# Optimization experiments

Measured on AMD Instinct MI355X. Metric: run time of the kernel, lower is better.

Reference implementation:

```python
import jax, jax.numpy as jnp
import numpy as np

B, S, E, H = 2, 2048, 1024, 16
D = E // H  # head dim = 64


def setup_inputs() -> dict:
    key = jax.random.key(0)
    ks = jax.random.split(key, 9)
    sc = 0.02
    return {
        "inputs": jax.random.normal(ks[0], (B, S, E), jnp.float32),
        "Wq": jax.random.normal(ks[1], (E, E), jnp.float32) * sc,
        "bq": jnp.zeros((E,), jnp.float32),
        "Wk": jax.random.normal(ks[2], (E, E), jnp.float32) * sc,
        "bk": jnp.zeros((E,), jnp.float32),
        "Wv": jax.random.normal(ks[3], (E, E), jnp.float32) * sc,
        "bv": jnp.zeros((E,), jnp.float32),
        "Wo": jax.random.normal(ks[4], (E, E), jnp.float32) * sc,
        "bo": jnp.zeros((E,), jnp.float32),
    }


def _split_heads(x):
    # [B, S, E] -> [B, H, S, D]
    b, s, _ = x.shape
    return x.reshape(b, s, H, D).transpose(0, 2, 1, 3)


def reference(inputs, Wq, bq, Wk, bk, Wv, bv, Wo, bo):
    q = _split_heads(inputs @ Wq + bq)
    k = _split_heads(inputs @ Wk + bk)
    v = _split_heads(inputs @ Wv + bv)

    # scaled dot-product scores: [B, H, S, S]
    score = jnp.einsum("bhqd,bhkd->bhqk", q, k) / jnp.sqrt(jnp.float32(D))

    # causal mask, exactly as the original: score*mask - 10000*(1-mask)
    i = jnp.arange(S)[:, None]
    j = jnp.arange(S)[None, :]
    mask = (i >= j).astype(score.dtype)  # square case of i >= j - S + S
    score = score * mask - 10000.0 * (1.0 - mask)

    weights = jax.nn.softmax(score, axis=-1)
    attn = jnp.einsum("bhqk,bhkd->bhqd", weights, v)  # [B, H, S, D]
    attn = attn.transpose(0, 2, 1, 3).reshape(inputs.shape[0], S, E)
    return attn @ Wo + bo
```

## Files before the change

### kernel.cpp

```cpp
#include <hip/hip_runtime.h>
#include <stdint.h>

#define Bc 2
#define Sc 2048
#define Ec 1024
#define Hc 16
#define Dc 64
#define Mc (Bc*Sc)

typedef __attribute__((ext_vector_type(4))) float f32x4;
typedef __attribute__((ext_vector_type(8))) short bf16x8v;

#define SCL 0.1803368801f

__device__ __forceinline__ unsigned short f2bf(float f){
  unsigned int u = __float_as_uint(f);
  u += 0x7FFFu + ((u >> 16) & 1u);
  return (unsigned short)(u >> 16);
}

#define GLDS(src, dst) __builtin_amdgcn_global_load_lds( \
    (const __attribute__((address_space(1))) void*)(src), \
    (__attribute__((address_space(3))) void*)(dst), 16, 0, 0)

__global__ __launch_bounds__(256) void k_prep(const float* __restrict__ X,
                                              unsigned short* __restrict__ Xb,
                                              const float* __restrict__ W0, const float* __restrict__ W1,
                                              const float* __restrict__ W2, const float* __restrict__ W3,
                                              unsigned short* __restrict__ WT4){
  __shared__ float st[64][65];
  int bx = blockIdx.x, t = threadIdx.x;
  if (bx < 4096){
    int i = bx*256 + t;
    float4 v = ((const float4*)X)[i];
    ushort4 o;
    o.x = f2bf(v.x); o.y = f2bf(v.y); o.z = f2bf(v.z); o.w = f2bf(v.w);
    ((ushort4*)Xb)[i] = o;
  } else {
    int id = bx - 4096;
    int z = id >> 8, rem = id & 255;
    int k0 = (rem >> 4)*64, n0 = (rem & 15)*64;
    const float* W = (z==0)?W0 : (z==1)?W1 : (z==2)?W2 : W3;
    unsigned short* o = WT4 + (size_t)z * Ec * Ec;
    #pragma unroll
    for (int i=0;i<16;i++){ int lin=i*256+t; int r=lin>>6, c=lin&63;
      st[r][c] = W[(size_t)(k0+r)*Ec + n0+c]; }
    __syncthreads();
    #pragma unroll
    for (int i=0;i<16;i++){ int lin=i*256+t; int nn=lin>>6, kk=lin&63;
      o[(size_t)(n0+nn)*Ec + k0+kk] = f2bf(st[kk][nn]); }
  }
}

__global__ __launch_bounds__(256,2) void k_qkv(const unsigned short* __restrict__ A,
                                               const unsigned short* __restrict__ WT4,
                                               const float* __restrict__ bq,
                                               const float* __restrict__ bk,
                                               const float* __restrict__ bv,
                                               unsigned short* __restrict__ QKV){
  __shared__ unsigned short sA[2][128*64];
  __shared__ unsigned short sB[2][3][64*64];
  int bm = blockIdx.y, bn = blockIdx.x;
  int t = threadIdx.x, w = t>>6, lane = t&63, quad = lane>>4, m16 = lane&15;
  int wm = w>>1, wn = w&1, sw = m16 & 7;
  f32x4 acc[3][4][2];
  #pragma unroll
  for (int z=0;z<3;z++)
    #pragma unroll
    for (int i=0;i<4;i++)
      #pragma unroll
      for (int j=0;j<2;j++) acc[z][i][j] = (f32x4){0.f,0.f,0.f,0.f};

  auto stage = [&](int kt, int buf){
    #pragma unroll
    for (int i=0;i<4;i++){
      int cb = (w*4 + i)*64;
      int L = cb + lane;
      int row = L>>3, c = (L&7) ^ (row&7);
      GLDS(A + (size_t)(bm*128 + row)*Ec + kt*64 + c*8, &sA[buf][0] + cb*8);
    }
    #pragma unroll
    for (int z=0;z<3;z++)
      #pragma unroll
      for (int i=0;i<2;i++){
        int cb = (w*2 + i)*64;
        int L = cb + lane;
        int row = L>>3, c = (L&7) ^ (row&7);
        GLDS(WT4 + (size_t)z*Ec*Ec + (size_t)(bn*64 + row)*Ec + kt*64 + c*8,
             &sB[buf][z][0] + cb*8);
      }
  };

  stage(0, 0);
  for (int kt=0; kt<Ec/64; ++kt){
    int cur = kt & 1;
    __syncthreads();
    if (kt+1 < Ec/64) stage(kt+1, cur^1);
    bf16x8v af[4][2];
    #pragma unroll
    for (int s=0;s<4;s++){
      int row = wm*64 + s*16 + m16;
      af[s][0] = *(const bf16x8v*)(&sA[cur][0] + row*64 + ((quad  )^sw)*8);
      af[s][1] = *(const bf16x8v*)(&sA[cur][0] + row*64 + ((quad+4)^sw)*8);
    }
    #pragma unroll
    for (int z=0;z<3;z++){
      bf16x8v bfr[2][2];
      #pragma unroll
      for (int sn=0;sn<2;sn++){
        int rowb = wn*32 + sn*16 + m16;
        bfr[sn][0] = *(const bf16x8v*)(&sB[cur][z][0] + rowb*64 + ((quad  )^sw)*8);
        bfr[sn][1] = *(const bf16x8v*)(&sB[cur][z][0] + rowb*64 + ((quad+4)^sw)*8);
      }
      #pragma unroll
      for (int sm=0;sm<4;sm++)
        #pragma unroll
        for (int sn=0;sn<2;sn++){
          acc[z][sm][sn] = __builtin_amdgcn_mfma_f32_16x16x32_bf16(af[sm][0], bfr[sn][0], acc[z][sm][sn], 0,0,0);
          acc[z][sm][sn] = __builtin_amdgcn_mfma_f32_16x16x32_bf16(af[sm][1], bfr[sn][1], acc[z][sm][sn], 0,0,0);
        }
    }
  }
  #pragma unroll
  for (int z=0;z<3;z++){
    const float* bias = (z==0)?bq : (z==1)?bk : bv;
    unsigned short* Out = QKV + (size_t)z * (size_t)Mc * Ec;
    #pragma unroll
    for (int sm=0;sm<4;sm++){
      int row0 = bm*128 + wm*64 + sm*16 + quad*4;
      int bidx = row0 >> 11;
      #pragma unroll
      for (int sn=0;sn<2;sn++){
        int col = bn*64 + wn*32 + sn*16 + m16;
        float bb = bias[col];
        int h = col >> 6, d = col & 63;
        if (z == 2){
          int s0 = row0 & (Sc-1);
          ushort4 pk;
          pk.x = f2bf(acc[z][sm][sn][0] + bb);
          pk.y = f2bf(acc[z][sm][sn][1] + bb);
          pk.z = f2bf(acc[z][sm][sn][2] + bb);
          pk.w = f2bf(acc[z][sm][sn][3] + bb);
          *(ushort4*)(Out + (((size_t)bidx*Hc + h)*Dc + d)*Sc + s0) = pk;
        } else {
          float sc_ = (z==0) ? SCL : 1.0f;
          #pragma unroll
          for (int r=0;r<4;r++){
            int s = (row0 + r) & (Sc-1);
            Out[(((size_t)bidx*Hc + h)*Sc + s)*Dc + d] = f2bf((acc[z][sm][sn][r] + bb)*sc_);
          }
        }
      }
    }
  }
}

__global__ __launch_bounds__(256,2) void k_gemm1(const unsigned short* __restrict__ A,
                                                 const unsigned short* __restrict__ WT,
                                                 const float* __restrict__ bias,
                                                 float* __restrict__ Out){
  __shared__ unsigned short sA[2][128*64];
  __shared__ unsigned short sB[2][64*64];
  int bm = blockIdx.y, bn = blockIdx.x;
  int t = threadIdx.x, w = t>>6, lane = t&63, quad = lane>>4, m16 = lane&15;
  int wm = w>>1, wn = w&1, sw = m16 & 7;
  f32x4 acc[4][2];
  #pragma unroll
  for (int i=0;i<4;i++)
    #pragma unroll
    for (int j=0;j<2;j++) acc[i][j] = (f32x4){0.f,0.f,0.f,0.f};

  auto stage = [&](int kt, int buf){
    #pragma unroll
    for (int i=0;i<4;i++){
      int cb = (w*4 + i)*64;
      int L = cb + lane;
      int row = L>>3, c = (L&7) ^ (row&7);
      GLDS(A + (size_t)(bm*128 + row)*Ec + kt*64 + c*8, &sA[buf][0] + cb*8);
    }
    #pragma unroll
    for (int i=0;i<2;i++){
      int cb = (w*2 + i)*64;
      int L = cb + lane;
      int row = L>>3, c = (L&7) ^ (row&7);
      GLDS(WT + (size_t)(bn*64 + row)*Ec + kt*64 + c*8, &sB[buf][0] + cb*8);
    }
  };

  stage(0, 0);
  for (int kt=0; kt<Ec/64; ++kt){
    int cur = kt & 1;
    __syncthreads();
    if (kt+1 < Ec/64) stage(kt+1, cur^1);
    bf16x8v af[4][2], bfr[2][2];
    #pragma unroll
    for (int s=0;s<4;s++){
      int row = wm*64 + s*16 + m16;
      af[s][0] = *(const bf16x8v*)(&sA[cur][0] + row*64 + ((quad  )^sw)*8);
      af[s][1] = *(const bf16x8v*)(&sA[cur][0] + row*64 + ((quad+4)^sw)*8);
    }
    #pragma unroll
    for (int sn=0;sn<2;sn++){
      int rowb = wn*32 + sn*16 + m16;
      bfr[sn][0] = *(const bf16x8v*)(&sB[cur][0] + rowb*64 + ((quad  )^sw)*8);
      bfr[sn][1] = *(const bf16x8v*)(&sB[cur][0] + rowb*64 + ((quad+4)^sw)*8);
    }
    #pragma unroll
    for (int sm=0;sm<4;sm++)
      #pragma unroll
      for (int sn=0;sn<2;sn++){
        acc[sm][sn] = __builtin_amdgcn_mfma_f32_16x16x32_bf16(af[sm][0], bfr[sn][0], acc[sm][sn], 0,0,0);
        acc[sm][sn] = __builtin_amdgcn_mfma_f32_16x16x32_bf16(af[sm][1], bfr[sn][1], acc[sm][sn], 0,0,0);
      }
  }
  #pragma unroll
  for (int sm=0;sm<4;sm++){
    int row0 = bm*128 + wm*64 + sm*16 + quad*4;
    #pragma unroll
    for (int sn=0;sn<2;sn++){
      int col = bn*64 + wn*32 + sn*16 + m16;
      float bb = bias[col];
      #pragma unroll
      for (int r=0;r<4;r++)
        Out[(size_t)(row0+r)*Ec + col] = acc[sm][sn][r] + bb;
    }
  }
}

__device__ __forceinline__ void attn_tile(const unsigned short* sK, const unsigned short* sVT,
                                          unsigned short* pw, bf16x8v qf0, bf16x8v qf1,
                                          bf16x8v ones, f32x4& li, f32x4* Oa,
                                          int kbase, int qw, int quad, int m16){
  int sw = m16 & 7;
  f32x4 sc[4];
  #pragma unroll
  for (int sm=0;sm<4;sm++){
    int row = sm*16 + m16;
    bf16x8v kf0 = *(const bf16x8v*)(sK + row*64 + ((quad  )^sw)*8);
    bf16x8v kf1 = *(const bf16x8v*)(sK + row*64 + ((quad+4)^sw)*8);
    f32x4 a = (f32x4){0.f,0.f,0.f,0.f};
    a = __builtin_amdgcn_mfma_f32_16x16x32_bf16(kf0, qf0, a, 0,0,0);
    a = __builtin_amdgcn_mfma_f32_16x16x32_bf16(kf1, qf1, a, 0,0,0);
    sc[sm] = a;
  }
  if (kbase + 63 > qw){
    #pragma unroll
    for (int sm=0;sm<4;sm++)
      #pragma unroll
      for (int r=0;r<4;r++){
        int kg = kbase + sm*16 + quad*4 + r;
        float p = exp2f(sc[sm][r]);
        sc[sm][r] = (kg <= qw + m16) ? p : 0.0f;
      }
  } else {
    #pragma unroll
    for (int sm=0;sm<4;sm++)
      #pragma unroll
      for (int r=0;r<4;r++) sc[sm][r] = exp2f(sc[sm][r]);
  }

  #pragma unroll
  for (int sm=0;sm<4;sm++){
    ushort4 pk;
    pk.x = f2bf(sc[sm][0]); pk.y = f2bf(sc[sm][1]);
    pk.z = f2bf(sc[sm][2]); pk.w = f2bf(sc[sm][3]);
    int chunk = sm*2 + (quad>>1);
    *(ushort4*)(pw + m16*64 + (chunk^sw)*8 + (quad&1)*4) = pk;
  }
  bf16x8v pf0 = *(const bf16x8v*)(pw + m16*64 + ((quad  )^sw)*8);
  bf16x8v pf1 = *(const bf16x8v*)(pw + m16*64 + ((quad+4)^sw)*8);

  li = __builtin_amdgcn_mfma_f32_16x16x32_bf16(pf0, ones, li, 0,0,0);
  li = __builtin_amdgcn_mfma_f32_16x16x32_bf16(pf1, ones, li, 0,0,0);

  #pragma unroll
  for (int tt=0;tt<4;tt++){
    int rowv = tt*16 + m16;
    bf16x8v vf0 = *(const bf16x8v*)(sVT + rowv*64 + ((quad  )^sw)*8);
    bf16x8v vf1 = *(const bf16x8v*)(sVT + rowv*64 + ((quad+4)^sw)*8);
    Oa[tt] = __builtin_amdgcn_mfma_f32_16x16x32_bf16(pf0, vf0, Oa[tt], 0,0,0);
    Oa[tt] = __builtin_amdgcn_mfma_f32_16x16x32_bf16(pf1, vf1, Oa[tt], 0,0,0);
  }
}

__global__ __launch_bounds__(256,2) void k_attn(const unsigned short* __restrict__ Qb,
                                                const unsigned short* __restrict__ Kb,
                                                const unsigned short* __restrict__ VTb,
                                                unsigned short* __restrict__ Ob){
  __shared__ unsigned short sK [2][64*64];
  __shared__ unsigned short sVT[2][64*64];
  __shared__ unsigned short sP [4][16*64];
  int bh = blockIdx.y;
  int qtA = (int)blockIdx.x;
  int qtB = 31 - qtA;
  size_t base = (size_t)bh * Sc * Dc;
  const unsigned short* Q  = Qb  + base;
  const unsigned short* K  = Kb  + base;
  const unsigned short* VT = VTb + base;
  int t = threadIdx.x, w = t>>6, lane = t&63, quad = lane>>4, m16 = lane&15;
  int qwA = qtA*64 + w*16;
  int qwB = qtB*64 + w*16;

  bf16x8v qA0 = *(const bf16x8v*)(Q + (size_t)(qwA + m16)*Dc + quad*8);
  bf16x8v qA1 = *(const bf16x8v*)(Q + (size_t)(qwA + m16)*Dc + 32 + quad*8);
  bf16x8v qB0 = *(const bf16x8v*)(Q + (size_t)(qwB + m16)*Dc + quad*8);
  bf16x8v qB1 = *(const bf16x8v*)(Q + (size_t)(qwB + m16)*Dc + 32 + quad*8);

  bf16x8v ones;
  #pragma unroll
  for (int i=0;i<8;i++) ones[i] = (short)0x3F80;

  f32x4 OaA[4], OaB[4];
  #pragma unroll
  for (int i=0;i<4;i++){ OaA[i] = (f32x4){0.f,0.f,0.f,0.f}; OaB[i] = (f32x4){0.f,0.f,0.f,0.f}; }
  f32x4 liA = (f32x4){0.f,0.f,0.f,0.f}, liB = (f32x4){0.f,0.f,0.f,0.f};

  unsigned short* pw = &sP[w][0];

  auto stage = [&](int kt, int buf){
    int kbase = kt*64;
    #pragma unroll
    for (int i=0;i<2;i++){
      int cb = (w*2 + i)*64;
      int L = cb + lane;
      int row = L>>3, p = L&7, c = p ^ (row&7);
      GLDS(K  + (size_t)(kbase+row)*Dc + c*8,        &sK[buf][0]  + cb*8);
      GLDS(VT + (size_t)row*Sc + kbase + c*8,        &sVT[buf][0] + cb*8);
    }
  };

  for (int kt=0; kt<=qtB; kt+=2){
    stage(kt, 0);
    bool have2 = (kt+1 <= qtB);
    if (have2) stage(kt+1, 1);
    __syncthreads();

    if (kt <= qtA)
      attn_tile(&sK[0][0], &sVT[0][0], pw, qA0, qA1, ones, liA, OaA, kt*64, qwA, quad, m16);
    attn_tile(&sK[0][0], &sVT[0][0], pw, qB0, qB1, ones, liB, OaB, kt*64, qwB, quad, m16);
    if (have2){
      if (kt+1 <= qtA)
        attn_tile(&sK[1][0], &sVT[1][0], pw, qA0, qA1, ones, liA, OaA, (kt+1)*64, qwA, quad, m16);
      attn_tile(&sK[1][0], &sVT[1][0], pw, qB0, qB1, ones, liB, OaB, (kt+1)*64, qwB, quad, m16);
    }
    __syncthreads();
  }

  int b = bh >> 4, h = bh & 15;
  float iA[4], iB[4];
  #pragma unroll
  for (int r=0;r<4;r++){ iA[r] = 1.0f/liA[r]; iB[r] = 1.0f/liB[r]; }
  #pragma unroll
  for (int tt=0;tt<4;tt++)
    #pragma unroll
    for (int r=0;r<4;r++){
      int e = h*64 + tt*16 + m16;
      int sA_ = qwA + quad*4 + r;
      int sB_ = qwB + quad*4 + r;
      Ob[((size_t)b*Sc + sA_)*Ec + e] = f2bf(OaA[tt][r]*iA[r]);
      Ob[((size_t)b*Sc + sB_)*Ec + e] = f2bf(OaB[tt][r]*iB[r]);
    }
}

extern "C" void kernel_launch(void* const* d_in, const int* in_sizes, int n_in,
                              void* d_out, int out_size, void* d_ws, size_t ws_size,
                              hipStream_t stream){
  const float* X  = (const float*)d_in[0];
  const float* Wq = (const float*)d_in[1];
  const float* bq = (const float*)d_in[2];
  const float* Wk = (const float*)d_in[3];
  const float* bk = (const float*)d_in[4];
  const float* Wv = (const float*)d_in[5];
  const float* bv = (const float*)d_in[6];
  const float* Wo = (const float*)d_in[7];
  const float* bo = (const float*)d_in[8];

  uint8_t* ws = (uint8_t*)d_ws;
  unsigned short* Xb  = (unsigned short*)(ws);
  unsigned short* WT4 = (unsigned short*)(ws + (size_t)(8u<<20));
  unsigned short* QKV = (unsigned short*)(ws + (size_t)(16u<<20));
  unsigned short* ATT = (unsigned short*)(ws + (size_t)(40u<<20));

  k_prep<<<dim3(5120), 256, 0, stream>>>(X, Xb, Wq, Wk, Wv, Wo, WT4);
  k_qkv<<<dim3(16,32), 256, 0, stream>>>(Xb, WT4, bq, bk, bv, QKV);
  k_attn<<<dim3(16,32), 256, 0, stream>>>(QKV, QKV + (size_t)Mc*Ec, QKV + 2*(size_t)Mc*Ec, ATT);
  k_gemm1<<<dim3(16,32), 256, 0, stream>>>(ATT, WT4 + (size_t)3*Ec*Ec, bo, (float*)d_out);
}
```

Measured before the change: 182.9 us.

## Split paired causal query tiles into separate blocks, use fast exp and packed bf16 convert

```diff
diff --git a/kernel.cpp b/kernel.cpp
--- a/kernel.cpp
+++ b/kernel.cpp
@@ -17,6 +17,18 @@
   unsigned int u = __float_as_uint(f);
   u += 0x7FFFu + ((u >> 16) & 1u);
   return (unsigned short)(u >> 16);
+}
+
+__device__ __forceinline__ unsigned int cvt_pk_bf16(float a, float b){
+  unsigned int d;
+  asm("v_cvt_pk_bf16_f32 %0, %1, %2" : "=v"(d) : "v"(a), "v"(b));
+  return d;
+}
+
+__device__ __forceinline__ float fast_exp2(float x){
+  float r;
+  asm("v_exp_f32 %0, %1" : "=v"(r) : "v"(x));
+  return r;
 }
 
 #define GLDS(src, dst) __builtin_amdgcn_global_load_lds( \
@@ -249,23 +261,23 @@
       #pragma unroll
       for (int r=0;r<4;r++){
         int kg = kbase + sm*16 + quad*4 + r;
-        float p = exp2f(sc[sm][r]);
+        float p = fast_exp2(sc[sm][r]);
         sc[sm][r] = (kg <= qw + m16) ? p : 0.0f;
       }
   } else {
     #pragma unroll
     for (int sm=0;sm<4;sm++)
       #pragma unroll
-      for (int r=0;r<4;r++) sc[sm][r] = exp2f(sc[sm][r]);
+      for (int r=0;r<4;r++) sc[sm][r] = fast_exp2(sc[sm][r]);
   }
 
   #pragma unroll
   for (int sm=0;sm<4;sm++){
-    ushort4 pk;
-    pk.x = f2bf(sc[sm][0]); pk.y = f2bf(sc[sm][1]);
-    pk.z = f2bf(sc[sm][2]); pk.w = f2bf(sc[sm][3]);
+    uint2 pk;
+    pk.x = cvt_pk_bf16(sc[sm][0], sc[sm][1]);
+    pk.y = cvt_pk_bf16(sc[sm][2], sc[sm][3]);
     int chunk = sm*2 + (quad>>1);
-    *(ushort4*)(pw + m16*64 + (chunk^sw)*8 + (quad&1)*4) = pk;
+    *(uint2*)(pw + m16*64 + (chunk^sw)*8 + (quad&1)*4) = pk;
   }
   bf16x8v pf0 = *(const bf16x8v*)(pw + m16*64 + ((quad  )^sw)*8);
   bf16x8v pf1 = *(const bf16x8v*)(pw + m16*64 + ((quad+4)^sw)*8);
@@ -283,7 +295,7 @@
   }
 }
 
-__global__ __launch_bounds__(256,2) void k_attn(const unsigned short* __restrict__ Qb,
+__global__ __launch_bounds__(256,4) void k_attn(const unsigned short* __restrict__ Qb,
                                                 const unsigned short* __restrict__ Kb,
                                                 const unsigned short* __restrict__ VTb,
                                                 unsigned short* __restrict__ Ob){
@@ -291,29 +303,25 @@
   __shared__ unsigned short sVT[2][64*64];
   __shared__ unsigned short sP [4][16*64];
   int bh = blockIdx.y;
-  int qtA = (int)blockIdx.x;
-  int qtB = 31 - qtA;
+  int qt = (blockIdx.y & 8) ? (31 - (int)blockIdx.x) : (int)blockIdx.x;
   size_t base = (size_t)bh * Sc * Dc;
   const unsigned short* Q  = Qb  + base;
   const unsigned short* K  = Kb  + base;
   const unsigned short* VT = VTb + base;
   int t = threadIdx.x, w = t>>6, lane = t&63, quad = lane>>4, m16 = lane&15;
-  int qwA = qtA*64 + w*16;
-  int qwB = qtB*64 + w*16;
-
-  bf16x8v qA0 = *(const bf16x8v*)(Q + (size_t)(qwA + m16)*Dc + quad*8);
-  bf16x8v qA1 = *(const bf16x8v*)(Q + (size_t)(qwA + m16)*Dc + 32 + quad*8);
-  bf16x8v qB0 = *(const bf16x8v*)(Q + (size_t)(qwB + m16)*Dc + quad*8);
-  bf16x8v qB1 = *(const bf16x8v*)(Q + (size_t)(qwB + m16)*Dc + 32 + quad*8);
+  int qw = qt*64 + w*16;
+
+  bf16x8v q0 = *(const bf16x8v*)(Q + (size_t)(qw + m16)*Dc + quad*8);
+  bf16x8v q1 = *(const bf16x8v*)(Q + (size_t)(qw + m16)*Dc + 32 + quad*8);
 
   bf16x8v ones;
   #pragma unroll
   for (int i=0;i<8;i++) ones[i] = (short)0x3F80;
 
-  f32x4 OaA[4], OaB[4];
-  #pragma unroll
-  for (int i=0;i<4;i++){ OaA[i] = (f32x4){0.f,0.f,0.f,0.f}; OaB[i] = (f32x4){0.f,0.f,0.f,0.f}; }
-  f32x4 liA = (f32x4){0.f,0.f,0.f,0.f}, liB = (f32x4){0.f,0.f,0.f,0.f};
+  f32x4 Oa[4];
+  #pragma unroll
+  for (int i=0;i<4;i++) Oa[i] = (f32x4){0.f,0.f,0.f,0.f};
+  f32x4 li = (f32x4){0.f,0.f,0.f,0.f};
 
   unsigned short* pw = &sP[w][0];
 
@@ -329,36 +337,29 @@
     }
   };
 
-  for (int kt=0; kt<=qtB; kt+=2){
+  for (int kt=0; kt<=qt; kt+=2){
     stage(kt, 0);
-    bool have2 = (kt+1 <= qtB);
+    bool have2 = (kt+1 <= qt);
     if (have2) stage(kt+1, 1);
     __syncthreads();
 
-    if (kt <= qtA)
-      attn_tile(&sK[0][0], &sVT[0][0], pw, qA0, qA1, ones, liA, OaA, kt*64, qwA, quad, m16);
-    attn_tile(&sK[0][0], &sVT[0][0], pw, qB0, qB1, ones, liB, OaB, kt*64, qwB, quad, m16);
-    if (have2){
-      if (kt+1 <= qtA)
-        attn_tile(&sK[1][0], &sVT[1][0], pw, qA0, qA1, ones, liA, OaA, (kt+1)*64, qwA, quad, m16);
-      attn_tile(&sK[1][0], &sVT[1][0], pw, qB0, qB1, ones, liB, OaB, (kt+1)*64, qwB, quad, m16);
-    }
+    attn_tile(&sK[0][0], &sVT[0][0], pw, q0, q1, ones, li, Oa, kt*64, qw, quad, m16);
+    if (have2)
+      attn_tile(&sK[1][0], &sVT[1][0], pw, q0, q1, ones, li, Oa, (kt+1)*64, qw, quad, m16);
     __syncthreads();
   }
 
   int b = bh >> 4, h = bh & 15;
-  float iA[4], iB[4];
-  #pragma unroll
-  for (int r=0;r<4;r++){ iA[r] = 1.0f/liA[r]; iB[r] = 1.0f/liB[r]; }
+  float iv[4];
+  #pragma unroll
+  for (int r=0;r<4;r++) iv[r] = 1.0f/li[r];
   #pragma unroll
   for (int tt=0;tt<4;tt++)
     #pragma unroll
     for (int r=0;r<4;r++){
       int e = h*64 + tt*16 + m16;
-      int sA_ = qwA + quad*4 + r;
-      int sB_ = qwB + quad*4 + r;
-      Ob[((size_t)b*Sc + sA_)*Ec + e] = f2bf(OaA[tt][r]*iA[r]);
-      Ob[((size_t)b*Sc + sB_)*Ec + e] = f2bf(OaB[tt][r]*iB[r]);
+      int s = qw + quad*4 + r;
+      Ob[((size_t)b*Sc + s)*Ec + e] = f2bf(Oa[tt][r]*iv[r]);
     }
 }
 
@@ -383,6 +384,6 @@
 
   k_prep<<<dim3(5120), 256, 0, stream>>>(X, Xb, Wq, Wk, Wv, Wo, WT4);
   k_qkv<<<dim3(16,32), 256, 0, stream>>>(Xb, WT4, bq, bk, bv, QKV);
-  k_attn<<<dim3(16,32), 256, 0, stream>>>(QKV, QKV + (size_t)Mc*Ec, QKV + 2*(size_t)Mc*Ec, ATT);
+  k_attn<<<dim3(32,32), 256, 0, stream>>>(QKV, QKV + (size_t)Mc*Ec, QKV + 2*(size_t)Mc*Ec, ATT);
   k_gemm1<<<dim3(16,32), 256, 0, stream>>>(ATT, WT4 + (size_t)3*Ec*Ec, bo, (float*)d_out);
 }
```

Measured after the change: 169.6 us. -7.3%, faster.
